# Optimization experiments

Measured on AMD Instinct MI355X. Metric: run time of the kernel, lower is better.

The kernel has to match this reference:

```python
import jax, jax.numpy as jnp
import numpy as np

SEQ_LEN = 512
HID = 2048
VOCAB = 128
OUT = 2


def setup_inputs() -> dict:
    key = jax.random.key(0)
    ks = jax.random.split(key, 7)
    s = 1.0 / np.sqrt(HID)
    return {
        "inputs": jax.random.randint(ks[0], (SEQ_LEN,), 0, VOCAB),
        "hx": jnp.zeros((1, HID), jnp.float32),
        "emb": jax.random.normal(ks[1], (VOCAB, HID), jnp.float32) * s,
        "w_ih": jax.random.normal(ks[2], (3 * HID, HID), jnp.float32) * s,
        "w_hh": jax.random.normal(ks[3], (3 * HID, HID), jnp.float32) * s,
        "b_ih": jax.random.normal(ks[4], (3 * HID,), jnp.float32) * s,
        "b_hh": jax.random.normal(ks[5], (3 * HID,), jnp.float32) * s,
        "w_out": jax.random.normal(ks[6], (OUT, HID), jnp.float32) * s,
        "b_out": jnp.zeros((OUT,), jnp.float32),
    }


def reference(inputs, hx, emb, w_ih, w_hh, b_ih, b_hh, w_out, b_out):
    # embed: [L] -> [L, 1, H] (batch of 1, matching view(len, 1, -1))
    x = emb[inputs][:, None, :]

    def gru_step(h, xt):
        gi = xt @ w_ih.T + b_ih            # [1, 3H]
        gh = h @ w_hh.T + b_hh             # [1, 3H]
        i_r, i_z, i_n = jnp.split(gi, 3, axis=-1)
        h_r, h_z, h_n = jnp.split(gh, 3, axis=-1)
        r = jax.nn.sigmoid(i_r + h_r)
        z = jax.nn.sigmoid(i_z + h_z)
        n = jnp.tanh(i_n + r * h_n)
        h_new = (1.0 - z) * n + z * h
        return h_new, None

    h_final, _ = jax.lax.scan(gru_step, hx, x)
    logits = h_final @ w_out.T + b_out     # [1, OUT]
    return jax.nn.log_softmax(logits, axis=1)
```

## Files before the change

### kernel.cpp

```cpp
#include <hip/hip_runtime.h>

#define HID    2048
#define G3     6144
#define NVOCAB 128
#define SEQ    512
#define NBLK   256
#define FLAG_STRIDE 16

__device__ __forceinline__ float sigmoidf_(float x) {
  return 1.f / (1.f + __expf(-x));
}
__device__ __forceinline__ float tanhf_(float x) {
  const float ax = fabsf(x);
  const float e2 = __expf(-2.f * ax);
  return copysignf((1.f - e2) / (1.f + e2), x);
}

__global__ __launch_bounds__(256) void gi_precompute(
    const float* __restrict__ emb,
    const float* __restrict__ w_ih,
    const float* __restrict__ b_ih,
    float* __restrict__ GI) {
  __shared__ float sE[64][33];
  __shared__ float sW[64][33];

  const int j0 = blockIdx.x * 64;
  const int v0 = blockIdx.y * 64;
  const int tid = threadIdx.x;
  const int tx = tid & 15;
  const int ty = tid >> 4;
  const int r  = tid >> 3;
  const int c4 = (tid & 7) * 4;

  float acc[4][4] = {};

  for (int k0 = 0; k0 < HID; k0 += 32) {
    __syncthreads();
    float4 eA = *(const float4*)&emb [(size_t)(v0 + r)      * HID + k0 + c4];
    float4 eB = *(const float4*)&emb [(size_t)(v0 + r + 32) * HID + k0 + c4];
    float4 wA = *(const float4*)&w_ih[(size_t)(j0 + r)      * HID + k0 + c4];
    float4 wB = *(const float4*)&w_ih[(size_t)(j0 + r + 32) * HID + k0 + c4];
    sE[r][c4+0] = eA.x; sE[r][c4+1] = eA.y; sE[r][c4+2] = eA.z; sE[r][c4+3] = eA.w;
    sE[r+32][c4+0] = eB.x; sE[r+32][c4+1] = eB.y; sE[r+32][c4+2] = eB.z; sE[r+32][c4+3] = eB.w;
    sW[r][c4+0] = wA.x; sW[r][c4+1] = wA.y; sW[r][c4+2] = wA.z; sW[r][c4+3] = wA.w;
    sW[r+32][c4+0] = wB.x; sW[r+32][c4+1] = wB.y; sW[r+32][c4+2] = wB.z; sW[r+32][c4+3] = wB.w;
    __syncthreads();

    #pragma unroll
    for (int kk = 0; kk < 32; ++kk) {
      float e0 = sE[ty*4+0][kk], e1 = sE[ty*4+1][kk];
      float e2 = sE[ty*4+2][kk], e3 = sE[ty*4+3][kk];
      float w0 = sW[tx*4+0][kk], w1 = sW[tx*4+1][kk];
      float w2 = sW[tx*4+2][kk], w3 = sW[tx*4+3][kk];
      acc[0][0] += e0*w0; acc[0][1] += e0*w1; acc[0][2] += e0*w2; acc[0][3] += e0*w3;
      acc[1][0] += e1*w0; acc[1][1] += e1*w1; acc[1][2] += e1*w2; acc[1][3] += e1*w3;
      acc[2][0] += e2*w0; acc[2][1] += e2*w1; acc[2][2] += e2*w2; acc[2][3] += e2*w3;
      acc[3][0] += e3*w0; acc[3][1] += e3*w1; acc[3][2] += e3*w2; acc[3][3] += e3*w3;
    }
  }

  #pragma unroll
  for (int a = 0; a < 4; ++a)
    #pragma unroll
    for (int b = 0; b < 4; ++b) {
      const int j = j0 + tx*4 + b;
      GI[(size_t)(v0 + ty*4 + a) * G3 + j] = acc[a][b] + b_ih[j];
    }
}

__global__ __launch_bounds__(256, 1) void gru_reg(
    const float* __restrict__ GI,
    const float* __restrict__ Whh,
    const float* __restrict__ bhh,
    const int*   __restrict__ inputs,
    const float* __restrict__ wout,
    const float* __restrict__ bout,
    float* __restrict__ hbuf,
    unsigned* __restrict__ flags,
    float* __restrict__ out,
    const float* __restrict__ hx) {

  __shared__ int   s_inp[SEQ];
  __shared__ float s_h[HID];
  __shared__ float s_logits[2];

  const int tid  = threadIdx.x;
  const int lane = tid & 63;
  const int wv   = tid >> 6;
  const int i0 = blockIdx.x * 4 + wv;
  const int i1 = i0 + 1024;

  for (int k = tid; k < SEQ; k += 256) s_inp[k] = inputs[k];

  float w_r0[32], w_z0[32], w_n0[32], w_r1[32], w_z1[32], w_n1[32];
  {
    const float* pr0 = Whh + (size_t)i0 * HID;
    const float* pz0 = Whh + (size_t)(i0 + HID) * HID;
    const float* pn0 = Whh + (size_t)(i0 + 2*HID) * HID;
    const float* pr1 = Whh + (size_t)i1 * HID;
    const float* pz1 = Whh + (size_t)(i1 + HID) * HID;
    const float* pn1 = Whh + (size_t)(i1 + 2*HID) * HID;
    #pragma unroll
    for (int c = 0; c < 8; ++c) {
      const int k = c * 256 + lane * 4;
      *(float4*)&w_r0[c*4] = *(const float4*)&pr0[k];
      *(float4*)&w_z0[c*4] = *(const float4*)&pz0[k];
      *(float4*)&w_n0[c*4] = *(const float4*)&pn0[k];
      *(float4*)&w_r1[c*4] = *(const float4*)&pr1[k];
      *(float4*)&w_z1[c*4] = *(const float4*)&pz1[k];
      *(float4*)&w_n1[c*4] = *(const float4*)&pn1[k];
    }
  }
  #pragma unroll
  for (int c = 0; c < 32; ++c) {
    asm volatile("" : "+v"(w_r0[c]), "+v"(w_z0[c]), "+v"(w_n0[c]),
                      "+v"(w_r1[c]), "+v"(w_z1[c]), "+v"(w_n1[c]));
  }

  const float br0 = bhh[i0], bz0 = bhh[i0+HID], bn0 = bhh[i0+2*HID];
  const float br1 = bhh[i1], bz1 = bhh[i1+HID], bn1 = bhh[i1+2*HID];

  float* hb0 = hbuf;
  float* hb1 = hbuf + HID;
  __syncthreads();

  for (int t = 0; t < SEQ; ++t) {
    const int v = s_inp[t];
    const float* gi = GI + (size_t)v * G3;

    if (t == 0) {
      #pragma unroll
      for (int j = 0; j < 8; ++j) s_h[j*256 + tid] = hx[j*256 + tid];
    } else {
      const float* hr = (t & 1) ? hb0 : hb1;
      float tmp[8];
      #pragma unroll
      for (int j = 0; j < 8; ++j)
        tmp[j] = __hip_atomic_load(hr + j*256 + tid, __ATOMIC_RELAXED,
                                   __HIP_MEMORY_SCOPE_AGENT);
      #pragma unroll
      for (int j = 0; j < 8; ++j) s_h[j*256 + tid] = tmp[j];
    }
    __syncthreads();

    float ar0=0.f, az0=0.f, an0=0.f, ar1=0.f, az1=0.f, an1=0.f;
    #pragma unroll
    for (int c = 0; c < 8; ++c) {
      const float4 h4 = *(const float4*)&s_h[c*256 + lane*4];
      ar0 = fmaf(w_r0[c*4+0], h4.x, ar0); ar0 = fmaf(w_r0[c*4+1], h4.y, ar0);
      ar0 = fmaf(w_r0[c*4+2], h4.z, ar0); ar0 = fmaf(w_r0[c*4+3], h4.w, ar0);
      az0 = fmaf(w_z0[c*4+0], h4.x, az0); az0 = fmaf(w_z0[c*4+1], h4.y, az0);
      az0 = fmaf(w_z0[c*4+2], h4.z, az0); az0 = fmaf(w_z0[c*4+3], h4.w, az0);
      an0 = fmaf(w_n0[c*4+0], h4.x, an0); an0 = fmaf(w_n0[c*4+1], h4.y, an0);
      an0 = fmaf(w_n0[c*4+2], h4.z, an0); an0 = fmaf(w_n0[c*4+3], h4.w, an0);
      ar1 = fmaf(w_r1[c*4+0], h4.x, ar1); ar1 = fmaf(w_r1[c*4+1], h4.y, ar1);
      ar1 = fmaf(w_r1[c*4+2], h4.z, ar1); ar1 = fmaf(w_r1[c*4+3], h4.w, ar1);
      az1 = fmaf(w_z1[c*4+0], h4.x, az1); az1 = fmaf(w_z1[c*4+1], h4.y, az1);
      az1 = fmaf(w_z1[c*4+2], h4.z, az1); az1 = fmaf(w_z1[c*4+3], h4.w, az1);
      an1 = fmaf(w_n1[c*4+0], h4.x, an1); an1 = fmaf(w_n1[c*4+1], h4.y, an1);
      an1 = fmaf(w_n1[c*4+2], h4.z, an1); an1 = fmaf(w_n1[c*4+3], h4.w, an1);
    }

    const float gir0 = gi[i0], giz0 = gi[i0+HID], gin0 = gi[i0+2*HID];
    const float gir1 = gi[i1], giz1 = gi[i1+HID], gin1 = gi[i1+2*HID];
    const float hp0 = s_h[i0], hp1 = s_h[i1];

    #pragma unroll
    for (int m = 32; m > 0; m >>= 1) {
      ar0 += __shfl_xor(ar0, m); az0 += __shfl_xor(az0, m); an0 += __shfl_xor(an0, m);
      ar1 += __shfl_xor(ar1, m); az1 += __shfl_xor(az1, m); an1 += __shfl_xor(an1, m);
    }

    float* hw = (t & 1) ? hb1 : hb0;
    if (lane == 0) {
      const float r0 = sigmoidf_(gir0 + ar0 + br0);
      const float z0 = sigmoidf_(giz0 + az0 + bz0);
      const float n0 = tanhf_(gin0 + r0 * (an0 + bn0));
      __hip_atomic_store(hw + i0, (1.f - z0) * n0 + z0 * hp0,
                         __ATOMIC_RELAXED, __HIP_MEMORY_SCOPE_AGENT);
      const float r1 = sigmoidf_(gir1 + ar1 + br1);
      const float z1 = sigmoidf_(giz1 + az1 + bz1);
      const float n1 = tanhf_(gin1 + r1 * (an1 + bn1));
      __hip_atomic_store(hw + i1, (1.f - z1) * n1 + z1 * hp1,
                         __ATOMIC_RELAXED, __HIP_MEMORY_SCOPE_AGENT);
    }

    asm volatile("s_waitcnt vmcnt(0)" ::: "memory");
    __syncthreads();
    if (tid == 0)
      __hip_atomic_store(flags + blockIdx.x * FLAG_STRIDE, (unsigned)(t + 1),
                         __ATOMIC_RELAXED, __HIP_MEMORY_SCOPE_AGENT);
    while (__hip_atomic_load(flags + tid * FLAG_STRIDE,
                             __ATOMIC_RELAXED, __HIP_MEMORY_SCOPE_AGENT)
           != (unsigned)(t + 1))
      __builtin_amdgcn_s_sleep(1);
    __syncthreads();
  }

  if (blockIdx.x == 0) {
    const float* hf = hb1;
    if (wv < 2) {
      const float* wo = wout + (size_t)wv * HID;
      float acc = 0.f;
      #pragma unroll
      for (int c = 0; c < 32; ++c) {
        const int k = c * 64 + lane;
        const float hv = __hip_atomic_load(hf + k, __ATOMIC_RELAXED,
                                           __HIP_MEMORY_SCOPE_AGENT);
        acc = fmaf(wo[k], hv, acc);
      }
      #pragma unroll
      for (int m = 32; m > 0; m >>= 1) acc += __shfl_xor(acc, m);
      if (lane == 0) s_logits[wv] = acc + bout[wv];
    }
    __syncthreads();
    if (tid == 0) {
      const float l0 = s_logits[0], l1 = s_logits[1];
      const float mx = fmaxf(l0, l1);
      const float lse = mx + logf(expf(l0 - mx) + expf(l1 - mx));
      out[0] = l0 - lse;
      out[1] = l1 - lse;
    }
  }
}

__global__ __launch_bounds__(256) void gru_step_fb(
    const float* __restrict__ GI,
    const float* __restrict__ Whh,
    const float* __restrict__ bhh,
    const int*   __restrict__ inputs, int t,
    const float* __restrict__ h_in,
    float* __restrict__ h_out) {
  const int lane = threadIdx.x & 63;
  const int wvv  = threadIdx.x >> 6;
  const int i = blockIdx.x * 4 + wvv;
  const int v = inputs[t];

  const float4* hv = (const float4*)h_in;
  const float4* wr = (const float4*)(Whh + (size_t)i*HID);
  const float4* wz = (const float4*)(Whh + (size_t)(i+HID)*HID);
  const float4* wn = (const float4*)(Whh + (size_t)(i+2*HID)*HID);

  float ar=0.f, az=0.f, an=0.f;
  #pragma unroll
  for (int c = 0; c < 8; ++c) {
    const int idx = c*64 + lane;
    const float4 h4 = hv[idx];
    float4 a;
    a = wr[idx]; ar += a.x*h4.x + a.y*h4.y + a.z*h4.z + a.w*h4.w;
    a = wz[idx]; az += a.x*h4.x + a.y*h4.y + a.z*h4.z + a.w*h4.w;
    a = wn[idx]; an += a.x*h4.x + a.y*h4.y + a.z*h4.z + a.w*h4.w;
  }
  #pragma unroll
  for (int m = 32; m > 0; m >>= 1) {
    ar += __shfl_xor(ar, m); az += __shfl_xor(az, m); an += __shfl_xor(an, m);
  }
  if (lane == 0) {
    const float* gi = GI + (size_t)v * G3;
    const float r = sigmoidf_(gi[i] + ar + bhh[i]);
    const float z = sigmoidf_(gi[i+HID] + az + bhh[i+HID]);
    const float n = tanhf_(gi[i+2*HID] + r * (an + bhh[i+2*HID]));
    h_out[i] = (1.f - z) * n + z * h_in[i];
  }
}

__global__ void gru_out_fb(const float* __restrict__ h,
                           const float* __restrict__ wout,
                           const float* __restrict__ bout,
                           float* out) {
  __shared__ float logits[2];
  const int lane = threadIdx.x & 63;
  const int wvv  = threadIdx.x >> 6;
  if (wvv < 2) {
    const float4* wo = (const float4*)(wout + (size_t)wvv * HID);
    const float4* hv = (const float4*)h;
    float acc = 0.f;
    #pragma unroll
    for (int c = 0; c < 8; ++c) {
      const int idx = c*64 + lane;
      const float4 a  = wo[idx];
      const float4 h4 = hv[idx];
      acc += a.x*h4.x + a.y*h4.y + a.z*h4.z + a.w*h4.w;
    }
    #pragma unroll
    for (int m = 32; m > 0; m >>= 1) acc += __shfl_xor(acc, m);
    if (lane == 0) logits[wvv] = acc + bout[wvv];
  }
  __syncthreads();
  if (threadIdx.x == 0) {
    const float l0 = logits[0], l1 = logits[1];
    const float mx = fmaxf(l0, l1);
    const float lse = mx + logf(expf(l0 - mx) + expf(l1 - mx));
    out[0] = l0 - lse;
    out[1] = l1 - lse;
  }
}

extern "C" void kernel_launch(void* const* d_in, const int* in_sizes, int n_in,
                              void* d_out, int out_size, void* d_ws, size_t ws_size,
                              hipStream_t stream) {
  const int*   inputs = (const int*)  d_in[0];
  const float* hx     = (const float*)d_in[1];
  const float* emb    = (const float*)d_in[2];
  const float* w_ih   = (const float*)d_in[3];
  const float* w_hh   = (const float*)d_in[4];
  const float* b_ih   = (const float*)d_in[5];
  const float* b_hh   = (const float*)d_in[6];
  const float* w_out  = (const float*)d_in[7];
  const float* b_out  = (const float*)d_in[8];
  float* out = (float*)d_out;

  float*    GI    = (float*)d_ws;
  float*    hbuf  = GI + (size_t)NVOCAB * G3;
  unsigned* flags = (unsigned*)(hbuf + 2 * HID);

  gi_precompute<<<dim3(G3/64, NVOCAB/64), 256, 0, stream>>>(emb, w_ih, b_ih, GI);

  void* args[] = { (void*)&GI, (void*)&w_hh, (void*)&b_hh, (void*)&inputs,
                   (void*)&w_out, (void*)&b_out, (void*)&hbuf, (void*)&flags,
                   (void*)&out, (void*)&hx };
  hipError_t ce = hipLaunchCooperativeKernel((void*)gru_reg, dim3(NBLK), dim3(256),
                                             args, 0, stream);
  if (ce != hipSuccess) {
    float* h0 = hbuf;
    float* h1 = hbuf + HID;
    const float* hin = hx;
    for (int t = 0; t < SEQ; ++t) {
      float* hout = (t & 1) ? h1 : h0;
      gru_step_fb<<<512, 256, 0, stream>>>(GI, w_hh, b_hh, inputs, t, hin, hout);
      hin = hout;
    }
    gru_out_fb<<<1, 128, 0, stream>>>(hin, w_out, b_out, out);
  }
}
```

Baseline: 2.245 ms.

## Replace grid-wide flag barrier with tagged hidden-state words and prefetch GI

```diff
diff --git a/kernel.cpp b/kernel.cpp
--- a/kernel.cpp
+++ b/kernel.cpp
@@ -5,7 +5,7 @@
 #define NVOCAB 128
 #define SEQ    512
 #define NBLK   256
-#define FLAG_STRIDE 16
+#define TAGBASE 0x5EED0000u
 
 __device__ __forceinline__ float sigmoidf_(float x) {
   return 1.f / (1.f + __expf(-x));
@@ -75,8 +75,8 @@
     const int*   __restrict__ inputs,
     const float* __restrict__ wout,
     const float* __restrict__ bout,
-    float* __restrict__ hbuf,
-    unsigned* __restrict__ flags,
+    unsigned long long* __restrict__ bufU,
+    unsigned* __restrict__ done,
     float* __restrict__ out,
     const float* __restrict__ hx) {
 
@@ -89,6 +89,7 @@
   const int wv   = tid >> 6;
   const int i0 = blockIdx.x * 4 + wv;
   const int i1 = i0 + 1024;
+  unsigned* flag0 = done + 256 * 16;
 
   for (int k = tid; k < SEQ; k += 256) s_inp[k] = inputs[k];
 
@@ -113,35 +114,53 @@
   }
   #pragma unroll
   for (int c = 0; c < 32; ++c) {
-    asm volatile("" : "+v"(w_r0[c]), "+v"(w_z0[c]), "+v"(w_n0[c]),
-                      "+v"(w_r1[c]), "+v"(w_z1[c]), "+v"(w_n1[c]));
+    asm volatile("" : "+a"(w_r0[c]), "+a"(w_z0[c]), "+a"(w_n0[c]),
+                      "+a"(w_r1[c]), "+a"(w_z1[c]), "+a"(w_n1[c]));
   }
 
   const float br0 = bhh[i0], bz0 = bhh[i0+HID], bn0 = bhh[i0+2*HID];
   const float br1 = bhh[i1], bz1 = bhh[i1+HID], bn1 = bhh[i1+2*HID];
 
-  float* hb0 = hbuf;
-  float* hb1 = hbuf + HID;
   __syncthreads();
 
-  for (int t = 0; t < SEQ; ++t) {
-    const int v = s_inp[t];
-    const float* gi = GI + (size_t)v * G3;
-
-    if (t == 0) {
+  float g0r, g0z, g0n, g1r, g1z, g1n;
+  {
+    const float* gp = GI + (size_t)s_inp[0] * G3;
+    g0r = gp[i0]; g0z = gp[i0+HID]; g0n = gp[i0+2*HID];
+    g1r = gp[i1]; g1z = gp[i1+HID]; g1n = gp[i1+2*HID];
+  }
+
+  for (int s = 0; s < SEQ; ++s) {
+    if (s == 0) {
       #pragma unroll
       for (int j = 0; j < 8; ++j) s_h[j*256 + tid] = hx[j*256 + tid];
     } else {
-      const float* hr = (t & 1) ? hb0 : hb1;
-      float tmp[8];
-      #pragma unroll
-      for (int j = 0; j < 8; ++j)
-        tmp[j] = __hip_atomic_load(hr + j*256 + tid, __ATOMIC_RELAXED,
-                                   __HIP_MEMORY_SCOPE_AGENT);
-      #pragma unroll
-      for (int j = 0; j < 8; ++j) s_h[j*256 + tid] = tmp[j];
-    }
-    __syncthreads();
+      const unsigned wantTag = TAGBASE | (unsigned)s;
+      const unsigned long long* br_ = bufU + (size_t)(s & 1) * HID;
+      unsigned pending = 0xFFu;
+      while (pending) {
+        unsigned long long x[8];
+        #pragma unroll
+        for (int j = 0; j < 8; ++j)
+          if (pending & (1u << j))
+            x[j] = __hip_atomic_load(br_ + j*256 + tid, __ATOMIC_RELAXED,
+                                     __HIP_MEMORY_SCOPE_AGENT);
+        #pragma unroll
+        for (int j = 0; j < 8; ++j)
+          if ((pending & (1u << j)) && (unsigned)(x[j] >> 32) == wantTag) {
+            s_h[j*256 + tid] = __uint_as_float((unsigned)x[j]);
+            pending &= ~(1u << j);
+          }
+      }
+    }
+    __syncthreads();
+
+    float ng0r=g0r, ng0z=g0z, ng0n=g0n, ng1r=g1r, ng1z=g1z, ng1n=g1n;
+    if (s + 1 < SEQ) {
+      const float* gp = GI + (size_t)s_inp[s+1] * G3;
+      ng0r = gp[i0]; ng0z = gp[i0+HID]; ng0n = gp[i0+2*HID];
+      ng1r = gp[i1]; ng1z = gp[i1+HID]; ng1n = gp[i1+2*HID];
+    }
 
     float ar0=0.f, az0=0.f, an0=0.f, ar1=0.f, az1=0.f, an1=0.f;
     #pragma unroll
@@ -161,8 +180,6 @@
       an1 = fmaf(w_n1[c*4+2], h4.z, an1); an1 = fmaf(w_n1[c*4+3], h4.w, an1);
     }
 
-    const float gir0 = gi[i0], giz0 = gi[i0+HID], gin0 = gi[i0+2*HID];
-    const float gir1 = gi[i1], giz1 = gi[i1+HID], gin1 = gi[i1+2*HID];
     const float hp0 = s_h[i0], hp1 = s_h[i1];
 
     #pragma unroll
@@ -171,43 +188,64 @@
       ar1 += __shfl_xor(ar1, m); az1 += __shfl_xor(az1, m); an1 += __shfl_xor(an1, m);
     }
 
-    float* hw = (t & 1) ? hb1 : hb0;
     if (lane == 0) {
-      const float r0 = sigmoidf_(gir0 + ar0 + br0);
-      const float z0 = sigmoidf_(giz0 + az0 + bz0);
-      const float n0 = tanhf_(gin0 + r0 * (an0 + bn0));
-      __hip_atomic_store(hw + i0, (1.f - z0) * n0 + z0 * hp0,
-                         __ATOMIC_RELAXED, __HIP_MEMORY_SCOPE_AGENT);
-      const float r1 = sigmoidf_(gir1 + ar1 + br1);
-      const float z1 = sigmoidf_(giz1 + az1 + bz1);
-      const float n1 = tanhf_(gin1 + r1 * (an1 + bn1));
-      __hip_atomic_store(hw + i1, (1.f - z1) * n1 + z1 * hp1,
-                         __ATOMIC_RELAXED, __HIP_MEMORY_SCOPE_AGENT);
-    }
-
-    asm volatile("s_waitcnt vmcnt(0)" ::: "memory");
+      const unsigned tagv = TAGBASE | (unsigned)(s + 1);
+      unsigned long long* bw = bufU + (size_t)((s + 1) & 1) * HID;
+      const float r0 = sigmoidf_(g0r + ar0 + br0);
+      const float z0 = sigmoidf_(g0z + az0 + bz0);
+      const float n0 = tanhf_(g0n + r0 * (an0 + bn0));
+      const float h0n = (1.f - z0) * n0 + z0 * hp0;
+      const float r1 = sigmoidf_(g1r + ar1 + br1);
+      const float z1 = sigmoidf_(g1z + az1 + bz1);
+      const float n1 = tanhf_(g1n + r1 * (an1 + bn1));
+      const float h1n = (1.f - z1) * n1 + z1 * hp1;
+      __hip_atomic_store(bw + i0,
+          ((unsigned long long)tagv << 32) | (unsigned long long)__float_as_uint(h0n),
+          __ATOMIC_RELAXED, __HIP_MEMORY_SCOPE_AGENT);
+      __hip_atomic_store(bw + i1,
+          ((unsigned long long)tagv << 32) | (unsigned long long)__float_as_uint(h1n),
+          __ATOMIC_RELAXED, __HIP_MEMORY_SCOPE_AGENT);
+    }
+
+    g0r = ng0r; g0z = ng0z; g0n = ng0n;
+    g1r = ng1r; g1z = ng1z; g1n = ng1n;
+
+    __syncthreads();
+  }
+
+  if (blockIdx.x == 0) {
+    {
+      const unsigned wantTag = TAGBASE | (unsigned)SEQ;
+      const unsigned long long* br_ = bufU;
+      unsigned pending = 0xFFu;
+      while (pending) {
+        unsigned long long x[8];
+        #pragma unroll
+        for (int j = 0; j < 8; ++j)
+          if (pending & (1u << j))
+            x[j] = __hip_atomic_load(br_ + j*256 + tid, __ATOMIC_RELAXED,
+                                     __HIP_MEMORY_SCOPE_AGENT);
+        #pragma unroll
+        for (int j = 0; j < 8; ++j)
+          if ((pending & (1u << j)) && (unsigned)(x[j] >> 32) == wantTag) {
+            s_h[j*256 + tid] = __uint_as_float((unsigned)x[j]);
+            pending &= ~(1u << j);
+          }
+      }
+    }
     __syncthreads();
     if (tid == 0)
-      __hip_atomic_store(flags + blockIdx.x * FLAG_STRIDE, (unsigned)(t + 1),
-                         __ATOMIC_RELAXED, __HIP_MEMORY_SCOPE_AGENT);
-    while (__hip_atomic_load(flags + tid * FLAG_STRIDE,
-                             __ATOMIC_RELAXED, __HIP_MEMORY_SCOPE_AGENT)
-           != (unsigned)(t + 1))
-      __builtin_amdgcn_s_sleep(1);
-    __syncthreads();
-  }
-
-  if (blockIdx.x == 0) {
-    const float* hf = hb1;
+      __hip_atomic_store(flag0, 0xD0D0D0D0u, __ATOMIC_RELAXED,
+                         __HIP_MEMORY_SCOPE_AGENT);
+
     if (wv < 2) {
       const float* wo = wout + (size_t)wv * HID;
       float acc = 0.f;
       #pragma unroll
-      for (int c = 0; c < 32; ++c) {
-        const int k = c * 64 + lane;
-        const float hv = __hip_atomic_load(hf + k, __ATOMIC_RELAXED,
-                                           __HIP_MEMORY_SCOPE_AGENT);
-        acc = fmaf(wo[k], hv, acc);
+      for (int c = 0; c < 8; ++c) {
+        const float4 h4 = *(const float4*)&s_h[c*256 + lane*4];
+        const float4 a4 = *(const float4*)&wo[c*256 + lane*4];
+        acc += a4.x*h4.x + a4.y*h4.y + a4.z*h4.z + a4.w*h4.w;
       }
       #pragma unroll
       for (int m = 32; m > 0; m >>= 1) acc += __shfl_xor(acc, m);
@@ -221,6 +259,37 @@
       out[0] = l0 - lse;
       out[1] = l1 - lse;
     }
+    if (tid < 8) {
+      const int slot = (tid & 3) + (tid >> 2) * 1024;
+      __hip_atomic_store(bufU + slot, 0ull, __ATOMIC_RELAXED, __HIP_MEMORY_SCOPE_AGENT);
+      __hip_atomic_store(bufU + HID + slot, 0ull, __ATOMIC_RELAXED, __HIP_MEMORY_SCOPE_AGENT);
+    }
+    if (tid >= 1) {
+      while (__hip_atomic_load(done + tid * 16, __ATOMIC_RELAXED,
+                               __HIP_MEMORY_SCOPE_AGENT) != 0xD1D1D1D1u)
+        __builtin_amdgcn_s_sleep(8);
+    }
+    __syncthreads();
+    __hip_atomic_store(done + tid * 16, 0u, __ATOMIC_RELAXED, __HIP_MEMORY_SCOPE_AGENT);
+    if (tid == 0)
+      __hip_atomic_store(flag0, 0u, __ATOMIC_RELAXED, __HIP_MEMORY_SCOPE_AGENT);
+  } else {
+    if (tid == 0) {
+      while (__hip_atomic_load(flag0, __ATOMIC_RELAXED,
+                               __HIP_MEMORY_SCOPE_AGENT) != 0xD0D0D0D0u)
+        __builtin_amdgcn_s_sleep(8);
+    }
+    __syncthreads();
+    if (tid < 8) {
+      const int slot = blockIdx.x * 4 + (tid & 3) + (tid >> 2) * 1024;
+      __hip_atomic_store(bufU + slot, 0ull, __ATOMIC_RELAXED, __HIP_MEMORY_SCOPE_AGENT);
+      __hip_atomic_store(bufU + HID + slot, 0ull, __ATOMIC_RELAXED, __HIP_MEMORY_SCOPE_AGENT);
+    }
+    asm volatile("s_waitcnt vmcnt(0)" ::: "memory");
+    __syncthreads();
+    if (tid == 0)
+      __hip_atomic_store(done + blockIdx.x * 16, 0xD1D1D1D1u, __ATOMIC_RELAXED,
+                         __HIP_MEMORY_SCOPE_AGENT);
   }
 }
 
@@ -310,20 +379,21 @@
   const float* b_out  = (const float*)d_in[8];
   float* out = (float*)d_out;
 
-  float*    GI    = (float*)d_ws;
-  float*    hbuf  = GI + (size_t)NVOCAB * G3;
-  unsigned* flags = (unsigned*)(hbuf + 2 * HID);
+  float* GI = (float*)d_ws;
+  unsigned long long* bufU =
+      (unsigned long long*)((char*)d_ws + (size_t)NVOCAB * G3 * 4);
+  unsigned* done = (unsigned*)(bufU + 2 * HID);
 
   gi_precompute<<<dim3(G3/64, NVOCAB/64), 256, 0, stream>>>(emb, w_ih, b_ih, GI);
 
   void* args[] = { (void*)&GI, (void*)&w_hh, (void*)&b_hh, (void*)&inputs,
-                   (void*)&w_out, (void*)&b_out, (void*)&hbuf, (void*)&flags,
+                   (void*)&w_out, (void*)&b_out, (void*)&bufU, (void*)&done,
                    (void*)&out, (void*)&hx };
   hipError_t ce = hipLaunchCooperativeKernel((void*)gru_reg, dim3(NBLK), dim3(256),
                                              args, 0, stream);
   if (ce != hipSuccess) {
-    float* h0 = hbuf;
-    float* h1 = hbuf + HID;
+    float* h0 = (float*)bufU;
+    float* h1 = h0 + HID;
     const float* hin = hx;
     for (int t = 0; t < SEQ; ++t) {
       float* hout = (t & 1) ? h1 : h0;
```

Measured after the change: 2.239 ms. Within noise of the previous version (-0.3%).
